# Optimization experiments

Hardware: AMD Instinct MI355X
Metric: run time of the kernel (lower is better)

The kernel has to match this reference:

```python
import jax, jax.numpy as jnp
import numpy as np

HIDDEN = 2048
NUM_HEADS = 16
NUM_KV_HEADS = 8
HEAD_DIM = 128
EPS = 1e-6
ROPE_THETA = 10000.0
SEQ = 2048
Q_SIZE = NUM_HEADS * HEAD_DIM
KV_SIZE = NUM_KV_HEADS * HEAD_DIM


def rmsnorm_f32(x, w, eps=EPS):
    # RMSNormF32: normalize in float32, scale by weight
    xf = x.astype(jnp.float32)
    var = jnp.mean(xf * xf, axis=-1, keepdims=True)
    return xf * jax.lax.rsqrt(var + eps) * w.astype(jnp.float32)


def apply_rope(x, cos, sin):
    # x: [S, H, D]; cos/sin: [S, D//2] (neox-style half split)
    half = x.shape[-1] // 2
    x1, x2 = x[..., :half], x[..., half:]
    c = cos[:, None, :]
    s = sin[:, None, :]
    return jnp.concatenate([x1 * c - x2 * s, x2 * c + x1 * s], axis=-1)


def setup_inputs() -> dict:
    key = jax.random.key(0)
    ks = jax.random.split(key, 6)
    return {
        "positions": jnp.arange(SEQ, dtype=jnp.int32),
        "hidden_states": jax.random.normal(ks[0], (SEQ, HIDDEN), jnp.float32),
        "ln_weight": 1.0 + 0.1 * jax.random.normal(ks[1], (HIDDEN,), jnp.float32),
        "qkv_weight": 0.02 * jax.random.normal(ks[2], (Q_SIZE + 2 * KV_SIZE, HIDDEN), jnp.float32),
        "q_norm_weight": 1.0 + 0.1 * jax.random.normal(ks[3], (HEAD_DIM,), jnp.float32),
        "k_norm_weight": 1.0 + 0.1 * jax.random.normal(ks[4], (HEAD_DIM,), jnp.float32),
        "o_weight": 0.02 * jax.random.normal(ks[5], (HIDDEN, Q_SIZE), jnp.float32),
    }


def reference(positions, hidden_states, ln_weight, qkv_weight, q_norm_weight, k_norm_weight, o_weight):
    S = hidden_states.shape[0]
    # 1. input RMSNorm (f32)
    normalized = rmsnorm_f32(hidden_states, ln_weight)
    # 2. fused QKV projection (no bias)
    qkv = normalized @ qkv_weight.T  # [S, q_size + 2*kv_size]
    q = qkv[:, :Q_SIZE].reshape(S, NUM_HEADS, HEAD_DIM)
    k = qkv[:, Q_SIZE:Q_SIZE + KV_SIZE].reshape(S, NUM_KV_HEADS, HEAD_DIM)
    v = qkv[:, Q_SIZE + KV_SIZE:].reshape(S, NUM_KV_HEADS, HEAD_DIM)
    # 3. RoPE (neox half-split, cache built from theta)
    inv_freq = ROPE_THETA ** (-jnp.arange(0, HEAD_DIM, 2, dtype=jnp.float32) / HEAD_DIM)
    freqs = positions.astype(jnp.float32)[:, None] * inv_freq[None, :]  # [S, D/2]
    cos, sin = jnp.cos(freqs), jnp.sin(freqs)
    q = apply_rope(q, cos, sin)
    k = apply_rope(k, cos, sin)
    # 4. per-head q/k RMSNorm (applied after RoPE, as in source)
    q = rmsnorm_f32(q, q_norm_weight)
    k = rmsnorm_f32(k, k_norm_weight)
    # 5. GQA expand kv heads
    rep = NUM_HEADS // NUM_KV_HEADS
    k = jnp.repeat(k, rep, axis=1)  # [S, NH, D]
    v = jnp.repeat(v, rep, axis=1)
    # 6. naive causal attention
    scores = jnp.einsum('shd,thd->hst', q, k) / (HEAD_DIM ** 0.5)  # [NH, S, S]
    causal = jnp.triu(jnp.ones((S, S), dtype=bool), k=1)
    scores = jnp.where(causal[None, :, :], -jnp.inf, scores)
    attn = jax.nn.softmax(scores, axis=-1)
    attn = jnp.nan_to_num(attn, nan=0.0)
    out = jnp.einsum('hst,thd->shd', attn, v).reshape(S, Q_SIZE)
    # 7. output projection
    return out @ o_weight.T
```

## Files before the change

### kernel.cpp

```cpp
#include <hip/hip_runtime.h>
#include <hip/hip_bf16.h>
#include <stdint.h>

typedef unsigned short u16;
typedef __attribute__((ext_vector_type(4))) float f32x4;
typedef __attribute__((ext_vector_type(8))) __bf16 bf16x8;
typedef __attribute__((ext_vector_type(8))) unsigned short u16x8;
typedef __attribute__((ext_vector_type(4))) unsigned short u16x4;

#define SEQ 2048
#define HID 2048
#define HD  128

__device__ __forceinline__ float b2f(u16 v) {
    union { float f; unsigned u; } c; c.u = ((unsigned)v) << 16; return c.f;
}
__device__ __forceinline__ u16 f2b(float f) {
    union { float f; unsigned u; } c; c.f = f;
    unsigned r = c.u + 0x7fffu + ((c.u >> 16) & 1u);
    return (u16)(r >> 16);
}
__device__ __forceinline__ bf16x8 tob(u16x8 v) {
    union { u16x8 u; bf16x8 b; } c; c.u = v; return c.b;
}
__device__ __forceinline__ u16x8 ld8(const u16* p) { return *(const u16x8*)p; }

typedef const __attribute__((address_space(1))) unsigned int* gas_ptr;
typedef __attribute__((address_space(3))) unsigned int* las_ptr;
__device__ __forceinline__ void gld16(const void* g, void* l) {
    __builtin_amdgcn_global_load_lds((gas_ptr)g, (las_ptr)l, 16, 0, 0);
}

__global__ __launch_bounds__(256) void k_prep(const float* __restrict__ x,
                                              const float* __restrict__ w,
                                              u16* __restrict__ normed,
                                              const float* __restrict__ qkvw,
                                              u16* __restrict__ qkvwb) {
    const int b = blockIdx.x, t = threadIdx.x;
    if (b < 2048) {
        const int row = b;
        const float* xr = x + (size_t)row * HID + t * 8;
        f32x4 xa = *(const f32x4*)xr;
        f32x4 xb = *(const f32x4*)(xr + 4);
        float xf[8]; float ss = 0.f;
#pragma unroll
        for (int e = 0; e < 4; ++e) { xf[e] = xa[e]; xf[e + 4] = xb[e]; }
#pragma unroll
        for (int e = 0; e < 8; ++e) ss += xf[e] * xf[e];
#pragma unroll
        for (int m = 32; m; m >>= 1) ss += __shfl_xor(ss, m);
        __shared__ float red[4];
        if ((t & 63) == 0) red[t >> 6] = ss;
        __syncthreads();
        ss = red[0] + red[1] + red[2] + red[3];
        const float sc = rsqrtf(ss * (1.0f / HID) + 1e-6f);
        f32x4 wa = *(const f32x4*)(w + t * 8);
        f32x4 wb = *(const f32x4*)(w + t * 8 + 4);
        u16x8 ov;
#pragma unroll
        for (int e = 0; e < 4; ++e) {
            ov[e] = f2b(xf[e] * sc * wa[e]);
            ov[e + 4] = f2b(xf[e + 4] * sc * wb[e]);
        }
        *(u16x8*)(normed + (size_t)row * HID + t * 8) = ov;
    } else {
        const size_t i = ((size_t)(b - 2048) * 256 + t) * 8;
        f32x4 a = *(const f32x4*)(qkvw + i);
        f32x4 bb = *(const f32x4*)(qkvw + i + 4);
        u16x8 o;
#pragma unroll
        for (int e = 0; e < 4; ++e) { o[e] = f2b(a[e]); o[e + 4] = f2b(bb[e]); }
        *(u16x8*)(qkvwb + i) = o;
    }
}

__global__ __launch_bounds__(256) void k_conv(const float* __restrict__ src,
                                              u16* __restrict__ dst) {
    const size_t i = ((size_t)blockIdx.x * 256 + threadIdx.x) * 8;
    f32x4 a = *(const f32x4*)(src + i);
    f32x4 b = *(const f32x4*)(src + i + 4);
    u16x8 o;
#pragma unroll
    for (int e = 0; e < 4; ++e) { o[e] = f2b(a[e]); o[e + 4] = f2b(b[e]); }
    *(u16x8*)(dst + i) = o;
}

#define STAGE_G(buf, k0)                                                      \
    do {                                                                      \
        char* a0 = (char*)&As[buf][0][0] + wave * 1024;                       \
        char* a1 = (char*)&As[buf][1][0] + wave * 1024;                       \
        char* b0 = (char*)&Bs[buf][0][0] + wave * 1024;                       \
        char* b1 = (char*)&Bs[buf][1][0] + wave * 1024;                       \
        gld16(ga + (k0), a0);                                                 \
        gld16(ga + (k0) + rowskip, a0 + 4096);                                \
        gld16(ga + (k0) + 32, a1);                                            \
        gld16(ga + (k0) + 32 + rowskip, a1 + 4096);                           \
        gld16(gb + (k0), b0);                                                 \
        gld16(gb + (k0) + rowskip, b0 + 4096);                                \
        gld16(gb + (k0) + 32, b1);                                            \
        gld16(gb + (k0) + 32 + rowskip, b1 + 4096);                           \
    } while (0)

#define GEMM_PIPE(nk)                                                         \
    STAGE_G(0, 0);                                                            \
    for (int t = 0; t < (nk); ++t) {                                          \
        const int cur = t & 1;                                                \
        if (t + 1 < (nk)) {                                                   \
            STAGE_G(cur ^ 1, (t + 1) * 64);                                   \
            asm volatile("s_waitcnt vmcnt(8)" ::: "memory");                  \
        } else {                                                              \
            asm volatile("s_waitcnt vmcnt(0)" ::: "memory");                  \
        }                                                                     \
        __builtin_amdgcn_s_barrier();                                         \
        asm volatile("" ::: "memory");                                        \
        _Pragma("unroll")                                                     \
        for (int h = 0; h < 2; ++h) {                                         \
            const u16* as = &As[cur][h][0];                                   \
            const u16* bs = &Bs[cur][h][0];                                   \
            bf16x8 af[4], bfr[4];                                             \
            _Pragma("unroll")                                                 \
            for (int i = 0; i < 4; ++i)                                       \
                af[i] = tob(ld8(as + (wm * 64 + i * 16 + l16) * 32 + ((quad ^ sw) << 3))); \
            _Pragma("unroll")                                                 \
            for (int j = 0; j < 4; ++j)                                       \
                bfr[j] = tob(ld8(bs + (wn * 64 + j * 16 + l16) * 32 + ((quad ^ sw) << 3))); \
            _Pragma("unroll")                                                 \
            for (int i = 0; i < 4; ++i)                                       \
                _Pragma("unroll")                                             \
                for (int j = 0; j < 4; ++j)                                   \
                    acc[i][j] = __builtin_amdgcn_mfma_f32_16x16x32_bf16(af[i], bfr[j], acc[i][j], 0, 0, 0); \
        }                                                                     \
        asm volatile("" ::: "memory");                                        \
        __builtin_amdgcn_s_barrier();                                         \
    }

__global__ __launch_bounds__(256) void k_gemm_qkv(const u16* __restrict__ A,
                                                  const u16* __restrict__ B,
                                                  u16* __restrict__ qraw,
                                                  u16* __restrict__ kraw,
                                                  u16* __restrict__ vtr,
                                                  int K) {
    __shared__ u16 As[2][2][128 * 32];
    __shared__ u16 Bs[2][2][128 * 32];
    const int tid = threadIdx.x;
    const int wave = tid >> 6, lane = tid & 63, quad = lane >> 4, l16 = lane & 15;
    const int wm = wave >> 1, wn = wave & 1;
    const int sw = (l16 >> 1) & 3;
    const int m0 = blockIdx.x * 128, n0 = blockIdx.y * 128;
    f32x4 acc[4][4];
#pragma unroll
    for (int i = 0; i < 4; ++i)
#pragma unroll
        for (int j = 0; j < 4; ++j) acc[i][j] = (f32x4){0.f, 0.f, 0.f, 0.f};

    const int gchunk = (tid & 3) ^ ((tid >> 3) & 3);
    const u16* ga = A + (size_t)(m0 + (tid >> 2)) * K + gchunk * 8;
    const u16* gb = B + (size_t)(n0 + (tid >> 2)) * K + gchunk * 8;
    const size_t rowskip = (size_t)64 * K;

    GEMM_PIPE(K >> 6)

#pragma unroll
    for (int i = 0; i < 4; ++i) {
        const int row = m0 + wm * 64 + i * 16 + quad * 4;
#pragma unroll
        for (int j = 0; j < 4; ++j) {
            const int col = n0 + wn * 64 + j * 16 + l16;
#pragma unroll
            for (int r = 0; r < 4; ++r) {
                const u16 val = f2b(acc[i][j][r]);
                const int s = row + r;
                if (col < 2048) {
                    const int head = col >> 7, d = col & 127;
                    qraw[((size_t)head * SEQ + s) * HD + d] = val;
                } else if (col < 3072) {
                    const int c = col - 2048, kv = c >> 7, d = c & 127;
                    kraw[((size_t)kv * SEQ + s) * HD + d] = val;
                } else {
                    const int c = col - 3072, kv = c >> 7, d = c & 127;
                    vtr[(size_t)kv * HD * SEQ + (size_t)d * SEQ + s] = val;
                }
            }
        }
    }
}

__global__ __launch_bounds__(256) void k_gemm_of(const u16* __restrict__ A,
                                                 const u16* __restrict__ B,
                                                 float* __restrict__ P0,
                                                 float* __restrict__ P1,
                                                 int N, int K) {
    __shared__ u16 As[2][2][128 * 32];
    __shared__ u16 Bs[2][2][128 * 32];
    const int tid = threadIdx.x;
    const int wave = tid >> 6, lane = tid & 63, quad = lane >> 4, l16 = lane & 15;
    const int wm = wave >> 1, wn = wave & 1;
    const int sw = (l16 >> 1) & 3;
    const int m0 = blockIdx.x * 128, n0 = blockIdx.y * 128;
    const int kz = blockIdx.z;
    const int klen = K >> 1;
    f32x4 acc[4][4];
#pragma unroll
    for (int i = 0; i < 4; ++i)
#pragma unroll
        for (int j = 0; j < 4; ++j) acc[i][j] = (f32x4){0.f, 0.f, 0.f, 0.f};

    const int gchunk = (tid & 3) ^ ((tid >> 3) & 3);
    const u16* ga = A + (size_t)(m0 + (tid >> 2)) * K + gchunk * 8 + (size_t)kz * klen;
    const u16* gb = B + (size_t)(n0 + (tid >> 2)) * K + gchunk * 8 + (size_t)kz * klen;
    const size_t rowskip = (size_t)64 * K;

    GEMM_PIPE(klen >> 6)

    float* dst = kz ? P1 : P0;
#pragma unroll
    for (int i = 0; i < 4; ++i) {
        const int row = m0 + wm * 64 + i * 16 + quad * 4;
#pragma unroll
        for (int j = 0; j < 4; ++j) {
            const int col = n0 + wn * 64 + j * 16 + l16;
#pragma unroll
            for (int r = 0; r < 4; ++r)
                dst[(size_t)(row + r) * N + col] = acc[i][j][r];
        }
    }
}

__global__ __launch_bounds__(256) void k_ofmerge(const float* __restrict__ P0,
                                                 const float* __restrict__ P1,
                                                 float* __restrict__ C) {
    const size_t i = ((size_t)blockIdx.x * 256 + threadIdx.x) * 4;
    f32x4 a = *(const f32x4*)(P0 + i);
    f32x4 b = *(const f32x4*)(P1 + i);
#pragma unroll
    for (int e = 0; e < 4; ++e) a[e] += b[e];
    *(f32x4*)(C + i) = a;
}

__global__ __launch_bounds__(256) void k_ropenorm(const int* __restrict__ pos,
                                                  const float* __restrict__ qw,
                                                  const float* __restrict__ kw,
                                                  u16* __restrict__ qraw,
                                                  u16* __restrict__ kraw) {
    const int s = blockIdx.x;
    const int h = blockIdx.y * 4 + (threadIdx.x >> 6);
    const int d = threadIdx.x & 63;
    const bool isq = h < 16;
    u16* row = isq ? (qraw + ((size_t)h * SEQ + s) * HD)
                   : (kraw + ((size_t)(h - 16) * SEQ + s) * HD);
    const float x1 = b2f(row[d]), x2 = b2f(row[d + 64]);
    const float p = (float)pos[s];
    const float inv = exp2f(-(float)d * (2.0f / 128.0f) * 13.287712379549449f);
    const float fr = p * inv;
    const float c = cosf(fr), sn = sinf(fr);
    const float o1 = x1 * c - x2 * sn;
    const float o2 = x2 * c + x1 * sn;
    float ss = o1 * o1 + o2 * o2;
#pragma unroll
    for (int m = 32; m; m >>= 1) ss += __shfl_xor(ss, m);
    const float sc = rsqrtf(ss * (1.0f / HD) + 1e-6f);
    const float* w = isq ? qw : kw;
    row[d] = f2b(o1 * sc * w[d]);
    row[d + 64] = f2b(o2 * sc * w[d + 64]);
}

__global__ __launch_bounds__(256, 4) void k_attn(const u16* __restrict__ qh,
                                                 const u16* __restrict__ kh,
                                                 const u16* __restrict__ vt,
                                                 u16* __restrict__ out,
                                                 u16* __restrict__ po,
                                                 float* __restrict__ pl) {
    const int tid = threadIdx.x;
    const int wave = tid >> 6, lane = tid & 63, quad = lane >> 4, l16 = lane & 15;
    const int head = blockIdx.y;
    const int b = blockIdx.x;
    int qt, part, np;
    if (b < 11)      { qt = b;                      part = 0;            np = 1; }
    else if (b < 33) { qt = 11 + ((b - 11) >> 1);   part = (b - 11) & 1; np = 2; }
    else             { qt = 22 + (b - 33) / 3;      part = (b - 33) % 3; np = 3; }
    const int kvh = head >> 1;
    const int q0 = qt * 64;
    const int ntiles = qt + 1;

    __shared__ u16 Ks[64 * 128];
    __shared__ u16 Vts[128 * 64];
    __shared__ u16 Ps[4][16 * 64];

    const u16* qbase = qh + ((size_t)head * SEQ + q0 + wave * 16) * HD;
    bf16x8 aq[4];
#pragma unroll
    for (int kk = 0; kk < 4; ++kk)
        aq[kk] = tob(ld8(qbase + l16 * HD + kk * 32 + quad * 8));

    f32x4 acco[8];
#pragma unroll
    for (int j = 0; j < 8; ++j) acco[j] = (f32x4){0.f, 0.f, 0.f, 0.f};
    float lsum = 0.f;

    const float sc = 0.08838834764831845f;
    const u16* kbase = kh + (size_t)kvh * SEQ * HD;
    const u16* vbase = vt + (size_t)kvh * HD * SEQ;
    u16* pw = &Ps[wave][0];
    const int qrow_g = q0 + wave * 16 + l16;

    const u16* kg0 = kbase + (size_t)tid * 8;
    const u16* vg0 = vbase + (size_t)(tid >> 3) * SEQ + (size_t)(tid & 7) * 8;
    int kst[4], vst[4];
#pragma unroll
    for (int r = 0; r < 4; ++r) {
        const int krow = r * 16 + (tid >> 4);
        kst[r] = krow * 128 + (((tid & 15) ^ (krow & 7)) << 3);
        const int vrow = r * 32 + (tid >> 3);
        vst[r] = vrow * 64 + (((tid & 7) ^ (vrow & 7)) << 3);
    }

    u16x8 kreg[4], vreg[4];
    {
        const size_t koff = (size_t)part * 64;
#pragma unroll
        for (int r = 0; r < 4; ++r) {
            kreg[r] = ld8(kg0 + koff * HD + (size_t)r * 2048);
            vreg[r] = ld8(vg0 + koff + (size_t)r * 32 * SEQ);
        }
#pragma unroll
        for (int r = 0; r < 4; ++r) {
            *(u16x8*)(&Ks[0] + kst[r]) = kreg[r];
            *(u16x8*)(&Vts[0] + vst[r]) = vreg[r];
        }
    }
    __syncthreads();

    for (int kt = part; kt < ntiles; kt += np) {
        const bool havenext = (kt + np) < ntiles;
        if (havenext) {
            const size_t koff = (size_t)(kt + np) * 64;
#pragma unroll
            for (int r = 0; r < 4; ++r) {
                kreg[r] = ld8(kg0 + koff * HD + (size_t)r * 2048);
                vreg[r] = ld8(vg0 + koff + (size_t)r * 32 * SEQ);
            }
        }

        f32x4 accs[4];
#pragma unroll
        for (int j = 0; j < 4; ++j) accs[j] = (f32x4){0.f, 0.f, 0.f, 0.f};
#pragma unroll
        for (int kk = 0; kk < 4; ++kk) {
#pragma unroll
            for (int j = 0; j < 4; ++j) {
                const int krow = j * 16 + l16;
                const bf16x8 bk = tob(ld8(&Ks[0] + krow * 128 + (((kk * 4 + quad) ^ (krow & 7)) << 3)));
                accs[j] = __builtin_amdgcn_mfma_f32_16x16x32_bf16(bk, aq[kk], accs[j], 0, 0, 0);
            }
        }

        const int k0 = kt * 64;
#pragma unroll
        for (int j = 0; j < 4; ++j) {
            u16x4 pk;
#pragma unroll
            for (int r = 0; r < 4; ++r) {
                const int kpos = k0 + j * 16 + quad * 4 + r;
                const float pv = (kpos > qrow_g) ? 0.f : __expf(accs[j][r] * sc);
                lsum += pv;
                pk[r] = f2b(pv);
            }
            const int blk = (j * 2 + (quad >> 1)) ^ (l16 & 7);
            *(u16x4*)(pw + l16 * 64 + (blk << 3) + ((quad & 1) << 2)) = pk;
        }

#pragma unroll
        for (int kk = 0; kk < 2; ++kk) {
            const bf16x8 ap = tob(ld8(pw + l16 * 64 + (((kk * 4 + quad) ^ (l16 & 7)) << 3)));
#pragma unroll
            for (int j = 0; j < 8; ++j) {
                const int vrow = j * 16 + l16;
                const bf16x8 bv = tob(ld8(&Vts[0] + vrow * 64 + (((kk * 4 + quad) ^ (vrow & 7)) << 3)));
                acco[j] = __builtin_amdgcn_mfma_f32_16x16x32_bf16(ap, bv, acco[j], 0, 0, 0);
            }
        }

        __syncthreads();
        if (havenext) {
#pragma unroll
            for (int r = 0; r < 4; ++r) {
                *(u16x8*)(&Ks[0] + kst[r]) = kreg[r];
                *(u16x8*)(&Vts[0] + vst[r]) = vreg[r];
            }
        }
        __syncthreads();
    }

    float v = lsum;
    v += __shfl_xor(v, 16);
    v += __shfl_xor(v, 32);
    const int rowb = q0 + wave * 16 + quad * 4;

    if (np == 1) {
        f32x4 il;
#pragma unroll
        for (int r = 0; r < 4; ++r) il[r] = 1.0f / __shfl(v, quad * 4 + r);
#pragma unroll
        for (int j = 0; j < 8; ++j) {
            const int col = head * HD + j * 16 + l16;
#pragma unroll
            for (int r = 0; r < 4; ++r)
                out[(size_t)(rowb + r) * 2048 + col] = f2b(acco[j][r] * il[r]);
        }
    } else {
        u16* pob = po + (size_t)part * SEQ * 2048;
        float* plb = pl + (size_t)part * 16 * SEQ;
        if (lane < 16) plb[head * SEQ + q0 + wave * 16 + l16] = v;
#pragma unroll
        for (int j = 0; j < 8; ++j) {
            const int col = head * HD + j * 16 + l16;
#pragma unroll
            for (int r = 0; r < 4; ++r)
                pob[(size_t)(rowb + r) * 2048 + col] = f2b(acco[j][r]);
        }
    }
}

__global__ __launch_bounds__(256) void k_amerge(const u16* __restrict__ po,
                                                const float* __restrict__ pl,
                                                u16* __restrict__ out) {
    const int s = blockIdx.x + 704;
    const int qt = s >> 6;
    const int np = (qt > 21) ? 3 : 2;
    const int t = threadIdx.x;
    const int head = t >> 4;

    float l = 0.f;
#pragma unroll
    for (int p = 0; p < 3; ++p)
        if (p < np) l += pl[(size_t)p * 16 * SEQ + head * SEQ + s];
    const float il = 1.0f / l;

    float o[8] = {0.f, 0.f, 0.f, 0.f, 0.f, 0.f, 0.f, 0.f};
#pragma unroll
    for (int p = 0; p < 3; ++p) {
        if (p < np) {
            const u16x8 vv = ld8(po + (size_t)p * SEQ * 2048 + (size_t)s * 2048 + t * 8);
#pragma unroll
            for (int e = 0; e < 8; ++e) o[e] += b2f(vv[e]);
        }
    }
    u16x8 ov;
#pragma unroll
    for (int e = 0; e < 8; ++e) ov[e] = f2b(o[e] * il);
    *(u16x8*)(out + (size_t)s * 2048 + t * 8) = ov;
}

extern "C" void kernel_launch(void* const* d_in, const int* in_sizes, int n_in,
                              void* d_out, int out_size, void* d_ws, size_t ws_size,
                              hipStream_t stream) {
    const int*   positions = (const int*)d_in[0];
    const float* hidden   = (const float*)d_in[1];
    const float* lnw      = (const float*)d_in[2];
    const float* qkvw     = (const float*)d_in[3];
    const float* qnw      = (const float*)d_in[4];
    const float* knw      = (const float*)d_in[5];
    const float* ow       = (const float*)d_in[6];
    float* outp = (float*)d_out;

    char* ws = (char*)d_ws;
    const size_t MB = 1024ull * 1024ull;
    u16* normed = (u16*)(ws + 0 * MB);
    u16* qraw   = (u16*)(ws + 8 * MB);
    u16* kraw   = (u16*)(ws + 16 * MB);
    u16* vtr    = (u16*)(ws + 20 * MB);
    u16* qkvwb  = (u16*)(ws + 24 * MB);
    u16* owb    = (u16*)(ws + 0 * MB);
    u16* attno  = (u16*)(ws + 24 * MB);
    u16* po     = (u16*)(ws + 32 * MB);
    float* pl   = (float*)(ws + 56 * MB);
    float* ofp0 = (float*)(ws + 32 * MB);
    float* ofp1 = (float*)(ws + 8 * MB);

    k_prep    <<<6144, 256, 0, stream>>>(hidden, lnw, normed, qkvw, qkvwb);
    k_gemm_qkv<<<dim3(16, 32), 256, 0, stream>>>(normed, qkvwb, qraw, kraw, vtr, HID);
    k_ropenorm<<<dim3(SEQ, 6), 256, 0, stream>>>(positions, qnw, knw, qraw, kraw);
    k_conv    <<<2048, 256, 0, stream>>>(ow, owb);
    k_attn    <<<dim3(63, 16), 256, 0, stream>>>(qraw, kraw, vtr, attno, po, pl);
    k_amerge  <<<1344, 256, 0, stream>>>(po, pl, attno);
    k_gemm_of <<<dim3(16, 16, 2), 256, 0, stream>>>(attno, owb, ofp0, ofp1, HID, HID);
    k_ofmerge <<<4096, 256, 0, stream>>>(ofp0, ofp1, outp);
}
```

Measured before the change: 248.3 us.

## Replace split-K output GEMM with 128x64 tiles and fuse weight conversion into RoPE

The output projection no longer splits K into two partial products that a separate merge kernel sums. It now uses 128x64 tiles over the full K range, keeping a similar block count (512) and writing the final fp32 output directly. This drops the merge kernel and the round trip of partial results through memory. The o_weight bf16 conversion is also folded into the RoPE/norm kernel as an extra grid row, removing one more launch. The trade-offs are a longer K loop per block and lower arithmetic intensity per tile.

```diff
diff --git a/kernel.cpp b/kernel.cpp
--- a/kernel.cpp
+++ b/kernel.cpp
@@ -72,17 +72,6 @@
         for (int e = 0; e < 4; ++e) { o[e] = f2b(a[e]); o[e + 4] = f2b(bb[e]); }
         *(u16x8*)(qkvwb + i) = o;
     }
-}
-
-__global__ __launch_bounds__(256) void k_conv(const float* __restrict__ src,
-                                              u16* __restrict__ dst) {
-    const size_t i = ((size_t)blockIdx.x * 256 + threadIdx.x) * 8;
-    f32x4 a = *(const f32x4*)(src + i);
-    f32x4 b = *(const f32x4*)(src + i + 4);
-    u16x8 o;
-#pragma unroll
-    for (int e = 0; e < 4; ++e) { o[e] = f2b(a[e]); o[e + 4] = f2b(b[e]); }
-    *(u16x8*)(dst + i) = o;
 }
 
 #define STAGE_G(buf, k0)                                                      \
@@ -112,7 +101,7 @@
             asm volatile("s_waitcnt vmcnt(0)" ::: "memory");                  \
         }                                                                     \
         __builtin_amdgcn_s_barrier();                                         \
-        asm volatile("" ::: "memory");                                        \
+        asm volatile("" ::: "memory");                                       \
         _Pragma("unroll")                                                     \
         for (int h = 0; h < 2; ++h) {                                         \
             const u16* as = &As[cur][h][0];                                   \
@@ -130,8 +119,8 @@
                 for (int j = 0; j < 4; ++j)                                   \
                     acc[i][j] = __builtin_amdgcn_mfma_f32_16x16x32_bf16(af[i], bfr[j], acc[i][j], 0, 0, 0); \
         }                                                                     \
-        asm volatile("" ::: "memory");                                        \
-        __builtin_amdgcn_s_barrier();                                         \
+        asm volatile("" ::: "memory");                                       \
+        __builtin_amdgcn_s_barrier();                                        \
     }
 
 __global__ __launch_bounds__(256) void k_gemm_qkv(const u16* __restrict__ A,
@@ -187,81 +176,124 @@
 
 __global__ __launch_bounds__(256) void k_gemm_of(const u16* __restrict__ A,
                                                  const u16* __restrict__ B,
-                                                 float* __restrict__ P0,
-                                                 float* __restrict__ P1,
+                                                 float* __restrict__ C,
                                                  int N, int K) {
     __shared__ u16 As[2][2][128 * 32];
-    __shared__ u16 Bs[2][2][128 * 32];
+    __shared__ u16 Bs[2][2][64 * 32];
     const int tid = threadIdx.x;
     const int wave = tid >> 6, lane = tid & 63, quad = lane >> 4, l16 = lane & 15;
     const int wm = wave >> 1, wn = wave & 1;
     const int sw = (l16 >> 1) & 3;
-    const int m0 = blockIdx.x * 128, n0 = blockIdx.y * 128;
-    const int kz = blockIdx.z;
-    const int klen = K >> 1;
-    f32x4 acc[4][4];
+    const int m0 = blockIdx.x * 128, n0 = blockIdx.y * 64;
+    f32x4 acc[4][2];
 #pragma unroll
     for (int i = 0; i < 4; ++i)
 #pragma unroll
-        for (int j = 0; j < 4; ++j) acc[i][j] = (f32x4){0.f, 0.f, 0.f, 0.f};
+        for (int j = 0; j < 2; ++j) acc[i][j] = (f32x4){0.f, 0.f, 0.f, 0.f};
 
     const int gchunk = (tid & 3) ^ ((tid >> 3) & 3);
-    const u16* ga = A + (size_t)(m0 + (tid >> 2)) * K + gchunk * 8 + (size_t)kz * klen;
-    const u16* gb = B + (size_t)(n0 + (tid >> 2)) * K + gchunk * 8 + (size_t)kz * klen;
+    const u16* ga = A + (size_t)(m0 + (tid >> 2)) * K + gchunk * 8;
+    const u16* gb = B + (size_t)(n0 + (tid >> 2)) * K + gchunk * 8;
     const size_t rowskip = (size_t)64 * K;
 
-    GEMM_PIPE(klen >> 6)
-
-    float* dst = kz ? P1 : P0;
+#define STAGE_OF(buf, k0)                                                     \
+    do {                                                                      \
+        char* a0 = (char*)&As[buf][0][0] + wave * 1024;                       \
+        char* a1 = (char*)&As[buf][1][0] + wave * 1024;                       \
+        char* b0 = (char*)&Bs[buf][0][0] + wave * 1024;                       \
+        char* b1 = (char*)&Bs[buf][1][0] + wave * 1024;                       \
+        gld16(ga + (k0), a0);                                                 \
+        gld16(ga + (k0) + rowskip, a0 + 4096);                                \
+        gld16(ga + (k0) + 32, a1);                                            \
+        gld16(ga + (k0) + 32 + rowskip, a1 + 4096);                           \
+        gld16(gb + (k0), b0);                                                 \
+        gld16(gb + (k0) + 32, b1);                                            \
+    } while (0)
+
+    STAGE_OF(0, 0);
+    const int nk = K >> 6;
+    for (int t = 0; t < nk; ++t) {
+        const int cur = t & 1;
+        if (t + 1 < nk) {
+            STAGE_OF(cur ^ 1, (t + 1) * 64);
+            asm volatile("s_waitcnt vmcnt(6)" ::: "memory");
+        } else {
+            asm volatile("s_waitcnt vmcnt(0)" ::: "memory");
+        }
+        __builtin_amdgcn_s_barrier();
+        asm volatile("" ::: "memory");
+#pragma unroll
+        for (int h = 0; h < 2; ++h) {
+            const u16* as = &As[cur][h][0];
+            const u16* bs = &Bs[cur][h][0];
+            bf16x8 af[4], bfr[2];
+#pragma unroll
+            for (int i = 0; i < 4; ++i)
+                af[i] = tob(ld8(as + (wm * 64 + i * 16 + l16) * 32 + ((quad ^ sw) << 3)));
+#pragma unroll
+            for (int j = 0; j < 2; ++j)
+                bfr[j] = tob(ld8(bs + (wn * 32 + j * 16 + l16) * 32 + ((quad ^ sw) << 3)));
+#pragma unroll
+            for (int i = 0; i < 4; ++i)
+#pragma unroll
+                for (int j = 0; j < 2; ++j)
+                    acc[i][j] = __builtin_amdgcn_mfma_f32_16x16x32_bf16(af[i], bfr[j], acc[i][j], 0, 0, 0);
+        }
+        asm volatile("" ::: "memory");
+        __builtin_amdgcn_s_barrier();
+    }
+#undef STAGE_OF
+
 #pragma unroll
     for (int i = 0; i < 4; ++i) {
         const int row = m0 + wm * 64 + i * 16 + quad * 4;
 #pragma unroll
-        for (int j = 0; j < 4; ++j) {
-            const int col = n0 + wn * 64 + j * 16 + l16;
+        for (int j = 0; j < 2; ++j) {
+            const int col = n0 + wn * 32 + j * 16 + l16;
 #pragma unroll
             for (int r = 0; r < 4; ++r)
-                dst[(size_t)(row + r) * N + col] = acc[i][j][r];
-        }
-    }
-}
-
-__global__ __launch_bounds__(256) void k_ofmerge(const float* __restrict__ P0,
-                                                 const float* __restrict__ P1,
-                                                 float* __restrict__ C) {
-    const size_t i = ((size_t)blockIdx.x * 256 + threadIdx.x) * 4;
-    f32x4 a = *(const f32x4*)(P0 + i);
-    f32x4 b = *(const f32x4*)(P1 + i);
-#pragma unroll
-    for (int e = 0; e < 4; ++e) a[e] += b[e];
-    *(f32x4*)(C + i) = a;
-}
-
-__global__ __launch_bounds__(256) void k_ropenorm(const int* __restrict__ pos,
+                C[(size_t)(row + r) * N + col] = acc[i][j][r];
+        }
+    }
+}
+
+__global__ __launch_bounds__(256) void k_ropeconv(const int* __restrict__ pos,
                                                   const float* __restrict__ qw,
                                                   const float* __restrict__ kw,
                                                   u16* __restrict__ qraw,
-                                                  u16* __restrict__ kraw) {
-    const int s = blockIdx.x;
-    const int h = blockIdx.y * 4 + (threadIdx.x >> 6);
-    const int d = threadIdx.x & 63;
-    const bool isq = h < 16;
-    u16* row = isq ? (qraw + ((size_t)h * SEQ + s) * HD)
-                   : (kraw + ((size_t)(h - 16) * SEQ + s) * HD);
-    const float x1 = b2f(row[d]), x2 = b2f(row[d + 64]);
-    const float p = (float)pos[s];
-    const float inv = exp2f(-(float)d * (2.0f / 128.0f) * 13.287712379549449f);
-    const float fr = p * inv;
-    const float c = cosf(fr), sn = sinf(fr);
-    const float o1 = x1 * c - x2 * sn;
-    const float o2 = x2 * c + x1 * sn;
-    float ss = o1 * o1 + o2 * o2;
-#pragma unroll
-    for (int m = 32; m; m >>= 1) ss += __shfl_xor(ss, m);
-    const float sc = rsqrtf(ss * (1.0f / HD) + 1e-6f);
-    const float* w = isq ? qw : kw;
-    row[d] = f2b(o1 * sc * w[d]);
-    row[d + 64] = f2b(o2 * sc * w[d + 64]);
+                                                  u16* __restrict__ kraw,
+                                                  const float* __restrict__ ow,
+                                                  u16* __restrict__ owb) {
+    if (blockIdx.y < 6) {
+        const int s = blockIdx.x;
+        const int h = blockIdx.y * 4 + (threadIdx.x >> 6);
+        const int d = threadIdx.x & 63;
+        const bool isq = h < 16;
+        u16* row = isq ? (qraw + ((size_t)h * SEQ + s) * HD)
+                       : (kraw + ((size_t)(h - 16) * SEQ + s) * HD);
+        const float x1 = b2f(row[d]), x2 = b2f(row[d + 64]);
+        const float p = (float)pos[s];
+        const float inv = exp2f(-(float)d * (2.0f / 128.0f) * 13.287712379549449f);
+        const float fr = p * inv;
+        const float c = cosf(fr), sn = sinf(fr);
+        const float o1 = x1 * c - x2 * sn;
+        const float o2 = x2 * c + x1 * sn;
+        float ss = o1 * o1 + o2 * o2;
+#pragma unroll
+        for (int m = 32; m; m >>= 1) ss += __shfl_xor(ss, m);
+        const float sc = rsqrtf(ss * (1.0f / HD) + 1e-6f);
+        const float* w = isq ? qw : kw;
+        row[d] = f2b(o1 * sc * w[d]);
+        row[d + 64] = f2b(o2 * sc * w[d + 64]);
+    } else {
+        const size_t i = ((size_t)blockIdx.x * 256 + threadIdx.x) * 8;
+        f32x4 a = *(const f32x4*)(ow + i);
+        f32x4 b = *(const f32x4*)(ow + i + 4);
+        u16x8 o;
+#pragma unroll
+        for (int e = 0; e < 4; ++e) { o[e] = f2b(a[e]); o[e + 4] = f2b(b[e]); }
+        *(u16x8*)(owb + i) = o;
+    }
 }
 
 __global__ __launch_bounds__(256, 4) void k_attn(const u16* __restrict__ qh,
@@ -474,15 +506,11 @@
     u16* attno  = (u16*)(ws + 24 * MB);
     u16* po     = (u16*)(ws + 32 * MB);
     float* pl   = (float*)(ws + 56 * MB);
-    float* ofp0 = (float*)(ws + 32 * MB);
-    float* ofp1 = (float*)(ws + 8 * MB);
 
     k_prep    <<<6144, 256, 0, stream>>>(hidden, lnw, normed, qkvw, qkvwb);
     k_gemm_qkv<<<dim3(16, 32), 256, 0, stream>>>(normed, qkvwb, qraw, kraw, vtr, HID);
-    k_ropenorm<<<dim3(SEQ, 6), 256, 0, stream>>>(positions, qnw, knw, qraw, kraw);
-    k_conv    <<<2048, 256, 0, stream>>>(ow, owb);
+    k_ropeconv<<<dim3(SEQ, 7), 256, 0, stream>>>(positions, qnw, knw, qraw, kraw, ow, owb);
     k_attn    <<<dim3(63, 16), 256, 0, stream>>>(qraw, kraw, vtr, attno, po, pl);
     k_amerge  <<<1344, 256, 0, stream>>>(po, pl, attno);
-    k_gemm_of <<<dim3(16, 16, 2), 256, 0, stream>>>(attno, owb, ofp0, ofp1, HID, HID);
-    k_ofmerge <<<4096, 256, 0, stream>>>(ofp0, ofp1, outp);
-}
+    k_gemm_of <<<dim3(16, 32), 256, 0, stream>>>(attno, owb, outp, HID, HID);
+}
```

After: 246.7 us. No clear change (-0.6%).
